# Performance work log

Hardware: AMD Instinct MI355X
Metric: run time of the kernel (lower is better)

The kernel has to match this reference:

```python
import jax, jax.numpy as jnp
import numpy as np

RADIUS = 4
SIGMA_X = 5.0
SIGMA_I = 1.0


def gaussian_kernel3d():
    # norm.pdf(d)/norm.pdf(0) == exp(-d^2/2)
    r = RADIUS
    n = 2 * r + 1
    v = np.linspace(-r, r, n) ** 2
    xy, yz, zx = np.meshgrid(v, v, v)
    dist = (xy + yz + zx) / SIGMA_X
    k = np.exp(-0.5 * dist ** 2).astype(np.float32)  # (9,9,9)
    return jnp.asarray(k)


def setup_inputs() -> dict:
    key = jax.random.key(0)
    k1, k2 = jax.random.split(key)
    B, C, K, D, H, W = 2, 1, 5, 96, 96, 96
    inputs = jax.random.normal(k1, (B, C, D, H, W), jnp.float32)
    logits = jax.random.normal(k2, (B, K, D, H, W), jnp.float32)
    labels = jax.nn.softmax(logits, axis=1)  # class probabilities
    return {"inputs": inputs, "labels": labels}


def reference(inputs, labels):
    # inputs: [B,C,D,H,W] raw image; labels: [B,K,D,H,W] class probs
    K = labels.shape[1]
    kernel = gaussian_kernel3d()
    eps_m, eps_d = 1e-5, 1e-6

    # per-class, per-channel weighted mean: [B,K,C]
    num_mean = jnp.mean(inputs[:, None] * labels[:, :, None], axis=(3, 4, 5))
    den_mean = jnp.mean(labels, axis=(2, 3, 4))[..., None] + eps_m  # [B,K,1]
    class_mean = num_mean / den_mean  # [B,K,C]

    # diff: sum over channels of (x - mean)^2 -> [B,K,D,H,W]
    diff = jnp.sum((inputs[:, None] - class_mean[..., None, None, None]) ** 2, axis=2)
    weights = jnp.exp(-(diff ** 2) / (SIGMA_I ** 2))  # [B,K,D,H,W]

    # depthwise (per-class) 3D conv with the shared Gaussian kernel
    rhs = jnp.broadcast_to(kernel[None, None], (K, 1) + kernel.shape)  # [K,1,9,9,9]
    pad = [(RADIUS, RADIUS)] * 3

    def conv(x):  # x: [B,K,D,H,W]
        return jax.lax.conv_general_dilated(
            x, rhs, window_strides=(1, 1, 1), padding=pad,
            dimension_numbers=("NCDHW", "OIDHW", "NCDHW"),
            feature_group_count=K)

    numer = jnp.sum(labels * conv(labels * weights), axis=(0, 2, 3, 4))  # [K]
    denom = jnp.sum(labels * conv(weights), axis=(0, 2, 3, 4))  # [K]
    loss = jnp.sum(jnp.abs(numer / (denom + eps_d)))  # L1Loss vs zeros per class
    return jnp.asarray(K, inputs.dtype) - loss
```

## Files before the change

### kernel.cpp

```cpp
#include <hip/hip_runtime.h>
#include <math.h>

#define VOL (96*96*96)
#define KCLS 5
#define CZ 12
#define PSTR 56
#define PROWS 40
#define PSZ (PROWS*PSTR)
#define ZOFF (33*256)

typedef __attribute__((ext_vector_type(8))) short bf16x8;
typedef __attribute__((ext_vector_type(4))) float f32x4;
typedef __attribute__((ext_vector_type(4))) unsigned short us4;

__device__ __forceinline__ unsigned short f2bf(float f) {
  unsigned u = __builtin_bit_cast(unsigned, f);
  u += 0x7fffu + ((u >> 16) & 1u);
  return (unsigned short)(u >> 16);
}


__global__ __launch_bounds__(256) void k_sums(const float* __restrict__ I,
                                              const float* __restrict__ L,
                                              double* __restrict__ ws) {
  const int vol = blockIdx.y;
  const int b = vol / KCLS;
  const float4* __restrict__ I4 = (const float4*)(I + b * VOL);
  const float4* __restrict__ L4 = (const float4*)(L + vol * VOL);
  const int idx = blockIdx.x * 256 + threadIdx.x;
  float sL = 0.f, sIL = 0.f;
#pragma unroll
  for (int j = 0; j < 4; ++j) {
    float4 iv = I4[idx + j * 55296];
    float4 lv = L4[idx + j * 55296];
    sL += (lv.x + lv.y) + (lv.z + lv.w);
    sIL += iv.x * lv.x + iv.y * lv.y + iv.z * lv.z + iv.w * lv.w;
  }
#pragma unroll
  for (int off = 32; off; off >>= 1) {
    sL += __shfl_down(sL, off);
    sIL += __shfl_down(sIL, off);
  }
  __shared__ double red[8];
  const int wid = threadIdx.x >> 6;
  if ((threadIdx.x & 63) == 0) { red[wid] = (double)sL; red[4 + wid] = (double)sIL; }
  __syncthreads();
  if (threadIdx.x == 0) {
    atomicAdd(&ws[vol], red[0] + red[1] + red[2] + red[3]);
    atomicAdd(&ws[10 + vol], red[4] + red[5] + red[6] + red[7]);
  }
}

__global__ __launch_bounds__(256) void k_conv(const float* __restrict__ I,
                                              const float* __restrict__ L,
                                              double* __restrict__ ws) {
  __shared__ __attribute__((aligned(16))) short Atab[ZOFF + 8];
  __shared__ __attribute__((aligned(16))) short Wp[2][PSZ];
  __shared__ __attribute__((aligned(16))) short LWp[2][PSZ];
  __shared__ double red[8];

  const int t = threadIdx.x;
  const int vol = blockIdx.z;
  const int kcl = vol % KCLS;
  const int b = vol / KCLS;
  const int x0 = (blockIdx.x % 3) * 32;
  const int y0 = (blockIdx.x / 3) * 32;
  const int z0 = blockIdx.y * CZ;

  const float* __restrict__ Ib = I + b * VOL;
  const float* __restrict__ Lb = L + vol * VOL;

  const double sLd = ws[vol];
  const float mean = (float)(ws[10 + vol] / (sLd + 1e-5 * (double)VOL));

  for (int i = 0; i < 33; ++i) {
    const int idx = i * 256 + t;
    const int s2 = idx >> 8;
    const int rem = idx & 255;
    const int R = rem >> 3, j = rem & 7;
    const int dx = R - 15 + j;
    float val = 0.f;
    if (dx >= 0 && dx <= 8) {
      const float q = (float)(s2 + (dx - 4) * (dx - 4));
      val = __expf(-0.02f * q * q);
    }
    Atab[idx] = (short)f2bf(val);
  }
  if (t < 8) Atab[ZOFF + t] = 0;

  const int lane = t & 63;
  const int w = t >> 6;
  const int wx = w & 1, wy = w >> 1;
  const int nn = lane & 15, qq = lane >> 4;
  const int aBase = (qq < 3) ? ((8 * qq - nn + 15) * 8) : ZOFF;
  const int aMask = (qq < 3) ? -1 : 0;
  const int bBase = (16 * wy + nn) * PSTR + 16 * wx + 8 * qq;

  f32x4 accW[9], accL[9];
  const f32x4 zer = {0.f, 0.f, 0.f, 0.f};
#pragma unroll
  for (int i = 0; i < 9; ++i) { accW[i] = zer; accL[i] = zer; }
  float pN = 0.f, pD = 0.f;

  auto loadQuad = [&](int zp, int qi, float4& iv, float4& lv, bool& ok) {
    const int row = qi / 12;
    const int xq = (qi - row * 12) * 4;
    const int gy = y0 - 4 + row, gx = x0 - 4 + xq;
    ok = ((unsigned)zp < 96u) && ((unsigned)gy < 96u) && ((unsigned)gx <= 92u);
    if (ok) {
      const int off = (zp * 96 + gy) * 96 + gx;
      iv = *(const float4*)(Ib + off);
      lv = *(const float4*)(Lb + off);
    } else {
      iv = make_float4(0.f, 0.f, 0.f, 0.f);
      lv = make_float4(0.f, 0.f, 0.f, 0.f);
    }
  };
  auto storeQuad = [&](int buf, int qi, const float4& iv, const float4& lv, bool ok) {
    const int row = qi / 12;
    const int xq = (qi - row * 12) * 4;
    float d, w0, w1, w2, w3;
    d = iv.x - mean; d = d * d; w0 = ok ? __expf(-d * d) : 0.f;
    d = iv.y - mean; d = d * d; w1 = ok ? __expf(-d * d) : 0.f;
    d = iv.z - mean; d = d * d; w2 = ok ? __expf(-d * d) : 0.f;
    d = iv.w - mean; d = d * d; w3 = ok ? __expf(-d * d) : 0.f;
    us4 wv = { f2bf(w0), f2bf(w1), f2bf(w2), f2bf(w3) };
    us4 ov = { f2bf(lv.x * w0), f2bf(lv.y * w1), f2bf(lv.z * w2), f2bf(lv.w * w3) };
    *(us4*)(&Wp[buf][row * PSTR + xq]) = wv;
    *(us4*)(&LWp[buf][row * PSTR + xq]) = ov;
  };

  auto computePlane = [&](int buf, int zp) {
    const short* __restrict__ Wb = Wp[buf];
    const short* __restrict__ Lwb = LWp[buf];
    int iLo = z0 - (zp - 4); if (iLo < 0) iLo = 0;
    int iHi = (z0 + CZ - 1) - (zp - 4); if (iHi > 8) iHi = 8;
#pragma unroll 1
    for (int dy = 0; dy < 9; ++dy) {
      const int dy2 = (dy - 4) * (dy - 4);
      bf16x8 af[5];
#pragma unroll
      for (int da = 0; da < 5; ++da) {
        const int s2 = dy2 + da * da;
        af[da] = *(const bf16x8*)(Atab + aBase + ((s2 << 8) & aMask));
      }
      const int boff = bBase + dy * PSTR;
      const bf16x8 bw = *(const bf16x8*)(Wb + boff);
      const bf16x8 bl = *(const bf16x8*)(Lwb + boff);
#pragma unroll
      for (int i = 0; i < 9; ++i) {
        if (i >= iLo && i <= iHi) {
          const int da = (i < 4) ? (4 - i) : (i - 4);
          accW[i] = __builtin_amdgcn_mfma_f32_16x16x32_bf16(af[da], bw, accW[i], 0, 0, 0);
          accL[i] = __builtin_amdgcn_mfma_f32_16x16x32_bf16(af[da], bl, accL[i], 0, 0, 0);
        }
      }
    }
  };

  auto retire = [&](int zo) {
    if (zo >= z0 && zo < z0 + CZ) {
      const int gy = y0 + 16 * wy + nn;
      const int gx = x0 + 16 * wx + 4 * qq;
      const float4 lab = *(const float4*)(Lb + (zo * 96 + gy) * 96 + gx);
      pN += accL[0].x * lab.x + accL[0].y * lab.y + accL[0].z * lab.z + accL[0].w * lab.w;
      pD += accW[0].x * lab.x + accW[0].y * lab.y + accW[0].z * lab.z + accW[0].w * lab.w;
    }
#pragma unroll
    for (int i = 0; i < 8; ++i) { accW[i] = accW[i + 1]; accL[i] = accL[i + 1]; }
    accW[8] = zer; accL[8] = zer;
  };

  const int zp0 = z0 - 4;
  const int zend = z0 + CZ + 4;
  {
    float4 i0, l0, i1, l1; bool o0, o1;
    loadQuad(zp0, t, i0, l0, o0);
    storeQuad(0, t, i0, l0, o0);
    if (t < 224) { loadQuad(zp0, 256 + t, i1, l1, o1); storeQuad(0, 256 + t, i1, l1, o1); }
  }
  __syncthreads();

  for (int zp = zp0; zp < zend; ++zp) {
    const int cur = (zp - zp0) & 1;
    const bool more = (zp + 1 < zend);
    float4 i0, l0, i1, l1; bool o0 = false, o1 = false;
    if (more) {
      loadQuad(zp + 1, t, i0, l0, o0);
      if (t < 224) loadQuad(zp + 1, 256 + t, i1, l1, o1);
    }
    computePlane(cur, zp);
    retire(zp - 4);
    if (more) {
      storeQuad(cur ^ 1, t, i0, l0, o0);
      if (t < 224) storeQuad(cur ^ 1, 256 + t, i1, l1, o1);
    }
    __syncthreads();
  }

#pragma unroll
  for (int off = 32; off; off >>= 1) {
    pN += __shfl_down(pN, off);
    pD += __shfl_down(pD, off);
  }
  if (lane == 0) { red[w] = (double)pN; red[4 + w] = (double)pD; }
  __syncthreads();
  if (t == 0) {
    atomicAdd(&ws[20 + kcl], red[0] + red[1] + red[2] + red[3]);
    atomicAdd(&ws[25 + kcl], red[4] + red[5] + red[6] + red[7]);
  }
}

__global__ void k_final(const double* __restrict__ ws, float* __restrict__ out) {
  if (threadIdx.x == 0 && blockIdx.x == 0) {
    double loss = 0.0;
    for (int k = 0; k < KCLS; ++k) {
      loss += fabs(ws[20 + k] / (ws[25 + k] + 1e-6));
    }
    out[0] = (float)(5.0 - loss);
  }
}

extern "C" void kernel_launch(void* const* d_in, const int* in_sizes, int n_in,
                              void* d_out, int out_size, void* d_ws, size_t ws_size,
                              hipStream_t stream) {
  (void)in_sizes; (void)n_in; (void)out_size; (void)ws_size;
  const float* I = (const float*)d_in[0];
  const float* L = (const float*)d_in[1];
  double* ws = (double*)d_ws;
  float* out = (float*)d_out;

  hipMemsetAsync(d_ws, 0, 32 * sizeof(double), stream);
  k_sums<<<dim3(216, 10, 1), 256, 0, stream>>>(I, L, ws);
  k_conv<<<dim3(9, 8, 10), 256, 0, stream>>>(I, L, ws);
  k_final<<<1, 64, 0, stream>>>(ws, out);
}
```

Before: 196.4 us.

## Hoist Gaussian A-fragments into registers, swizzle LDS planes, fuse class sums

The conv kernel now builds a compact per-lane table of the 15 distinct squared-distance weight fragments, loads them once into registers, and selects them through a compile-time map, removing per-row LDS fragment loads. The plane buffers are padded to a 64 stride with an XOR swizzle to reduce LDS bank conflicts. Interior planes take a fully unrolled path with no per-slice range checks. The sums kernel reads each input chunk once and reuses it across all five classes. Register pressure rises and launch bounds now request two blocks per CU, which may cause spills.

```diff
diff --git a/kernel.cpp b/kernel.cpp
--- a/kernel.cpp
+++ b/kernel.cpp
@@ -4,14 +4,18 @@
 #define VOL (96*96*96)
 #define KCLS 5
 #define CZ 12
-#define PSTR 56
+#define PSTR 64
 #define PROWS 40
 #define PSZ (PROWS*PSTR)
-#define ZOFF (33*256)
+#define NS2 15
 
 typedef __attribute__((ext_vector_type(8))) short bf16x8;
 typedef __attribute__((ext_vector_type(4))) float f32x4;
 typedef __attribute__((ext_vector_type(4))) unsigned short us4;
+
+constexpr int S2VALS[NS2] = {0,1,2,4,5,8,9,10,13,16,17,18,20,25,32};
+constexpr int MAP33[33] = {0,1,2,-1,3,4,-1,-1,5,6,7,-1,-1,8,-1,-1,
+                           9,10,11,-1,12,-1,-1,-1,-1,13,-1,-1,-1,-1,-1,-1,14};
 
 __device__ __forceinline__ unsigned short f2bf(float f) {
   unsigned u = __builtin_bit_cast(unsigned, f);
@@ -23,38 +27,55 @@
 __global__ __launch_bounds__(256) void k_sums(const float* __restrict__ I,
                                               const float* __restrict__ L,
                                               double* __restrict__ ws) {
-  const int vol = blockIdx.y;
-  const int b = vol / KCLS;
+  const int b = blockIdx.y;
+  const int base = blockIdx.x * 2048 + threadIdx.x;
   const float4* __restrict__ I4 = (const float4*)(I + b * VOL);
-  const float4* __restrict__ L4 = (const float4*)(L + vol * VOL);
-  const int idx = blockIdx.x * 256 + threadIdx.x;
-  float sL = 0.f, sIL = 0.f;
-#pragma unroll
-  for (int j = 0; j < 4; ++j) {
-    float4 iv = I4[idx + j * 55296];
-    float4 lv = L4[idx + j * 55296];
-    sL += (lv.x + lv.y) + (lv.z + lv.w);
-    sIL += iv.x * lv.x + iv.y * lv.y + iv.z * lv.z + iv.w * lv.w;
-  }
-#pragma unroll
-  for (int off = 32; off; off >>= 1) {
-    sL += __shfl_down(sL, off);
-    sIL += __shfl_down(sIL, off);
-  }
-  __shared__ double red[8];
+  float4 iv[8];
+#pragma unroll
+  for (int j = 0; j < 8; ++j) iv[j] = I4[base + j * 256];
+  float sL[KCLS], sIL[KCLS];
+#pragma unroll
+  for (int k = 0; k < KCLS; ++k) { sL[k] = 0.f; sIL[k] = 0.f; }
+#pragma unroll 1
+  for (int k = 0; k < KCLS; ++k) {
+    const float4* __restrict__ L4 = (const float4*)(L + (b * KCLS + k) * VOL);
+#pragma unroll
+    for (int j = 0; j < 8; ++j) {
+      float4 lv = L4[base + j * 256];
+      sL[k] += (lv.x + lv.y) + (lv.z + lv.w);
+      sIL[k] += iv[j].x * lv.x + iv[j].y * lv.y + iv[j].z * lv.z + iv[j].w * lv.w;
+    }
+  }
+#pragma unroll
+  for (int k = 0; k < KCLS; ++k) {
+#pragma unroll
+    for (int off = 32; off; off >>= 1) {
+      sL[k] += __shfl_down(sL[k], off);
+      sIL[k] += __shfl_down(sIL[k], off);
+    }
+  }
+  __shared__ double red[4][2 * KCLS];
   const int wid = threadIdx.x >> 6;
-  if ((threadIdx.x & 63) == 0) { red[wid] = (double)sL; red[4 + wid] = (double)sIL; }
+  if ((threadIdx.x & 63) == 0) {
+#pragma unroll
+    for (int k = 0; k < KCLS; ++k) {
+      red[wid][k] = (double)sL[k];
+      red[wid][KCLS + k] = (double)sIL[k];
+    }
+  }
   __syncthreads();
-  if (threadIdx.x == 0) {
-    atomicAdd(&ws[vol], red[0] + red[1] + red[2] + red[3]);
-    atomicAdd(&ws[10 + vol], red[4] + red[5] + red[6] + red[7]);
-  }
-}
-
-__global__ __launch_bounds__(256) void k_conv(const float* __restrict__ I,
-                                              const float* __restrict__ L,
-                                              double* __restrict__ ws) {
-  __shared__ __attribute__((aligned(16))) short Atab[ZOFF + 8];
+  if (threadIdx.x < 2 * KCLS) {
+    double v = red[0][threadIdx.x] + red[1][threadIdx.x] + red[2][threadIdx.x] + red[3][threadIdx.x];
+    const int k = threadIdx.x % KCLS;
+    const int which = threadIdx.x / KCLS;
+    atomicAdd(&ws[(which ? 10 : 0) + b * KCLS + k], v);
+  }
+}
+
+__global__ __launch_bounds__(256, 2) void k_conv(const float* __restrict__ I,
+                                                 const float* __restrict__ L,
+                                                 double* __restrict__ ws) {
+  __shared__ __attribute__((aligned(16))) short AtabF[NS2 * 64 * 8];
   __shared__ __attribute__((aligned(16))) short Wp[2][PSZ];
   __shared__ __attribute__((aligned(16))) short LWp[2][PSZ];
   __shared__ double red[8];
@@ -73,28 +94,28 @@
   const double sLd = ws[vol];
   const float mean = (float)(ws[10 + vol] / (sLd + 1e-5 * (double)VOL));
 
-  for (int i = 0; i < 33; ++i) {
-    const int idx = i * 256 + t;
-    const int s2 = idx >> 8;
-    const int rem = idx & 255;
-    const int R = rem >> 3, j = rem & 7;
-    const int dx = R - 15 + j;
-    float val = 0.f;
-    if (dx >= 0 && dx <= 8) {
-      const float q = (float)(s2 + (dx - 4) * (dx - 4));
-      val = __expf(-0.02f * q * q);
-    }
-    Atab[idx] = (short)f2bf(val);
-  }
-  if (t < 8) Atab[ZOFF + t] = 0;
+#pragma unroll
+  for (int s2i = 0; s2i < NS2; ++s2i) {
+    const float s2c = (float)S2VALS[s2i];
+#pragma unroll
+    for (int h = 0; h < 2; ++h) {
+      const int sub = t + h * 256;
+      const int lane_ = sub >> 3;
+      const int j = sub & 7;
+      const int dx = ((lane_ >> 4) << 3) + j - (lane_ & 15);
+      float val = 0.f;
+      if (dx >= 0 && dx <= 8) {
+        const float q = s2c + (float)((dx - 4) * (dx - 4));
+        val = __expf(-0.02f * q * q);
+      }
+      AtabF[s2i * 512 + sub] = (short)f2bf(val);
+    }
+  }
 
   const int lane = t & 63;
   const int w = t >> 6;
   const int wx = w & 1, wy = w >> 1;
   const int nn = lane & 15, qq = lane >> 4;
-  const int aBase = (qq < 3) ? ((8 * qq - nn + 15) * 8) : ZOFF;
-  const int aMask = (qq < 3) ? -1 : 0;
-  const int bBase = (16 * wy + nn) * PSTR + 16 * wx + 8 * qq;
 
   f32x4 accW[9], accL[9];
   const f32x4 zer = {0.f, 0.f, 0.f, 0.f};
@@ -118,7 +139,9 @@
   };
   auto storeQuad = [&](int buf, int qi, const float4& iv, const float4& lv, bool ok) {
     const int row = qi / 12;
-    const int xq = (qi - row * 12) * 4;
+    const int q = qi - row * 12;
+    const int c = q >> 1, o = (q & 1) << 2;
+    const int a = row * PSTR + (((c ^ (row & 7)) << 3) + o);
     float d, w0, w1, w2, w3;
     d = iv.x - mean; d = d * d; w0 = ok ? __expf(-d * d) : 0.f;
     d = iv.y - mean; d = d * d; w1 = ok ? __expf(-d * d) : 0.f;
@@ -126,33 +149,59 @@
     d = iv.w - mean; d = d * d; w3 = ok ? __expf(-d * d) : 0.f;
     us4 wv = { f2bf(w0), f2bf(w1), f2bf(w2), f2bf(w3) };
     us4 ov = { f2bf(lv.x * w0), f2bf(lv.y * w1), f2bf(lv.z * w2), f2bf(lv.w * w3) };
-    *(us4*)(&Wp[buf][row * PSTR + xq]) = wv;
-    *(us4*)(&LWp[buf][row * PSTR + xq]) = ov;
-  };
-
-  auto computePlane = [&](int buf, int zp) {
+    *(us4*)(&Wp[buf][a]) = wv;
+    *(us4*)(&LWp[buf][a]) = ov;
+  };
+
+  {
+    float4 i0, l0, i1, l1; bool o0, o1;
+    loadQuad(z0 - 4, t, i0, l0, o0);
+    storeQuad(0, t, i0, l0, o0);
+    if (t < 224) { loadQuad(z0 - 4, 256 + t, i1, l1, o1); storeQuad(0, 256 + t, i1, l1, o1); }
+  }
+  __syncthreads();
+
+  bf16x8 afr[NS2];
+#pragma unroll
+  for (int r = 0; r < NS2; ++r)
+    afr[r] = *(const bf16x8*)(AtabF + (r * 64 + lane) * 8);
+
+  auto computeFull = [&](int buf) {
     const short* __restrict__ Wb = Wp[buf];
     const short* __restrict__ Lwb = LWp[buf];
-    int iLo = z0 - (zp - 4); if (iLo < 0) iLo = 0;
-    int iHi = (z0 + CZ - 1) - (zp - 4); if (iHi > 8) iHi = 8;
-#pragma unroll 1
+#pragma unroll
     for (int dy = 0; dy < 9; ++dy) {
-      const int dy2 = (dy - 4) * (dy - 4);
-      bf16x8 af[5];
-#pragma unroll
-      for (int da = 0; da < 5; ++da) {
-        const int s2 = dy2 + da * da;
-        af[da] = *(const bf16x8*)(Atab + aBase + ((s2 << 8) & aMask));
+      const int dy2c = (dy - 4) * (dy - 4);
+      const int yrow = 16 * wy + nn + dy;
+      const int boff = yrow * PSTR + ((((2 * wx + qq) ^ (yrow & 7))) << 3);
+      const bf16x8 bw = *(const bf16x8*)(Wb + boff);
+      const bf16x8 bl = *(const bf16x8*)(Lwb + boff);
+#pragma unroll
+      for (int i = 0; i < 9; ++i) {
+        const int da = (i < 4) ? (4 - i) : (i - 4);
+        const int ri = MAP33[dy2c + da * da];
+        accW[i] = __builtin_amdgcn_mfma_f32_16x16x32_bf16(afr[ri], bw, accW[i], 0, 0, 0);
+        accL[i] = __builtin_amdgcn_mfma_f32_16x16x32_bf16(afr[ri], bl, accL[i], 0, 0, 0);
       }
-      const int boff = bBase + dy * PSTR;
+    }
+  };
+  auto computeEdge = [&](int buf, int iLo, int iHi) {
+    const short* __restrict__ Wb = Wp[buf];
+    const short* __restrict__ Lwb = LWp[buf];
+#pragma unroll
+    for (int dy = 0; dy < 9; ++dy) {
+      const int dy2c = (dy - 4) * (dy - 4);
+      const int yrow = 16 * wy + nn + dy;
+      const int boff = yrow * PSTR + ((((2 * wx + qq) ^ (yrow & 7))) << 3);
       const bf16x8 bw = *(const bf16x8*)(Wb + boff);
       const bf16x8 bl = *(const bf16x8*)(Lwb + boff);
 #pragma unroll
       for (int i = 0; i < 9; ++i) {
         if (i >= iLo && i <= iHi) {
           const int da = (i < 4) ? (4 - i) : (i - 4);
-          accW[i] = __builtin_amdgcn_mfma_f32_16x16x32_bf16(af[da], bw, accW[i], 0, 0, 0);
-          accL[i] = __builtin_amdgcn_mfma_f32_16x16x32_bf16(af[da], bl, accL[i], 0, 0, 0);
+          const int ri = MAP33[dy2c + da * da];
+          accW[i] = __builtin_amdgcn_mfma_f32_16x16x32_bf16(afr[ri], bw, accW[i], 0, 0, 0);
+          accL[i] = __builtin_amdgcn_mfma_f32_16x16x32_bf16(afr[ri], bl, accL[i], 0, 0, 0);
         }
       }
     }
@@ -173,14 +222,6 @@
 
   const int zp0 = z0 - 4;
   const int zend = z0 + CZ + 4;
-  {
-    float4 i0, l0, i1, l1; bool o0, o1;
-    loadQuad(zp0, t, i0, l0, o0);
-    storeQuad(0, t, i0, l0, o0);
-    if (t < 224) { loadQuad(zp0, 256 + t, i1, l1, o1); storeQuad(0, 256 + t, i1, l1, o1); }
-  }
-  __syncthreads();
-
   for (int zp = zp0; zp < zend; ++zp) {
     const int cur = (zp - zp0) & 1;
     const bool more = (zp + 1 < zend);
@@ -189,7 +230,10 @@
       loadQuad(zp + 1, t, i0, l0, o0);
       if (t < 224) loadQuad(zp + 1, 256 + t, i1, l1, o1);
     }
-    computePlane(cur, zp);
+    int iLo = z0 - (zp - 4); if (iLo < 0) iLo = 0;
+    int iHi = (z0 + CZ - 1) - (zp - 4); if (iHi > 8) iHi = 8;
+    if (iLo == 0 && iHi == 8) computeFull(cur);
+    else computeEdge(cur, iLo, iHi);
     retire(zp - 4);
     if (more) {
       storeQuad(cur ^ 1, t, i0, l0, o0);
@@ -231,7 +275,7 @@
   float* out = (float*)d_out;
 
   hipMemsetAsync(d_ws, 0, 32 * sizeof(double), stream);
-  k_sums<<<dim3(216, 10, 1), 256, 0, stream>>>(I, L, ws);
+  k_sums<<<dim3(108, 2, 1), 256, 0, stream>>>(I, L, ws);
   k_conv<<<dim3(9, 8, 10), 256, 0, stream>>>(I, L, ws);
   k_final<<<1, 64, 0, stream>>>(ws, out);
 }
```

After: 192.1 us. -2.2%, faster.
